# Kernel tuning notes

Measured on AMD Instinct MI355X. Metric: run time of the kernel, lower is better.

The kernel has to match this reference:

```python
import jax, jax.numpy as jnp
import numpy as np

N_HEADS = 32
N_KV_HEADS = 8
HEAD_DIM = 128  # hidden 4096 / 32
NEG_INF = -1e9


def _apply_rope(x, cos, sin):
    # x: [B, S, H, D]; cos/sin: [S, D//2] -> complex multiply on (even, odd) pairs
    B, S, H, D = x.shape
    xr = x.reshape(B, S, H, D // 2, 2)
    a, b = xr[..., 0], xr[..., 1]
    c = cos[None, :, None, :]
    s = sin[None, :, None, :]
    out = jnp.stack([a * c - b * s, a * s + b * c], axis=-1)
    return out.reshape(B, S, H, D)


def setup_inputs() -> dict:
    key = jax.random.key(0)
    ks = jax.random.split(key, 8)
    B, S, HID = 1, 2048, 4096
    hidden_states = jax.random.normal(ks[0], (B, S, HID), dtype=jnp.float32)
    # causal additive mask [1,1,S,S]
    causal = jnp.tril(jnp.ones((S, S), dtype=bool))
    attention_mask = jnp.where(causal, 0.0, NEG_INF).astype(jnp.float32)[None, None]
    # true rotary frequencies (theta=500000 as in llama3)
    half = HEAD_DIM // 2
    inv_freq = 1.0 / (500000.0 ** (np.arange(0, half, dtype=np.float32) / half))
    angles = np.arange(S, dtype=np.float32)[:, None] * inv_freq[None, :]
    freqs_cos = jnp.asarray(np.cos(angles), dtype=jnp.float32)
    freqs_sin = jnp.asarray(np.sin(angles), dtype=jnp.float32)
    sc = 0.02
    wq = jax.random.normal(ks[1], (HID, HID), dtype=jnp.float32) * sc
    wk = jax.random.normal(ks[2], (N_KV_HEADS * HEAD_DIM, HID), dtype=jnp.float32) * sc
    wv = jax.random.normal(ks[3], (N_KV_HEADS * HEAD_DIM, HID), dtype=jnp.float32) * sc
    wo = jax.random.normal(ks[4], (HID, HID), dtype=jnp.float32) * sc
    return {"hidden_states": hidden_states, "attention_mask": attention_mask,
            "freqs_cos": freqs_cos, "freqs_sin": freqs_sin,
            "wq": wq, "wk": wk, "wv": wv, "wo": wo}


def reference(hidden_states, attention_mask, freqs_cos, freqs_sin, wq, wk, wv, wo):
    B, S, HID = hidden_states.shape
    n_rep = N_HEADS // N_KV_HEADS
    # projections (torch Linear: x @ W.T)
    q = (hidden_states @ wq.T).reshape(B, S, N_HEADS, HEAD_DIM)
    k = (hidden_states @ wk.T).reshape(B, S, N_KV_HEADS, HEAD_DIM)
    v = (hidden_states @ wv.T).reshape(B, S, N_KV_HEADS, HEAD_DIM)
    # rotary on q (full cos/sin) and k
    q = _apply_rope(q, freqs_cos, freqs_sin)
    k = _apply_rope(k, freqs_cos, freqs_sin)
    # [B, H, S, D]
    q = q.transpose(0, 2, 1, 3)
    k = k.transpose(0, 2, 1, 3)
    v = v.transpose(0, 2, 1, 3)
    # GQA: repeat_interleave kv heads
    k = jnp.repeat(k, n_rep, axis=1)
    v = jnp.repeat(v, n_rep, axis=1)
    scores = jnp.einsum("bhqd,bhkd->bhqk", q, k) / jnp.sqrt(jnp.float32(HEAD_DIM))
    scores = scores + attention_mask
    probs = jax.nn.softmax(scores.astype(jnp.float32), axis=-1)
    attn = jnp.einsum("bhqk,bhkd->bhqd", probs, v)
    attn = attn.transpose(0, 2, 1, 3).reshape(B, S, N_HEADS * HEAD_DIM)
    return attn @ wo.T
```

## Files before the change

### kernel.cpp

```cpp
#include <hip/hip_runtime.h>
#include <hip/hip_bf16.h>
#include <math.h>

#define SEQ 2048
#define HID 4096
#define NH 32
#define NKV 8
#define HD 128
#define KVG (NH / NKV)
#define NQKV 6144

typedef __bf16 bf16x8 __attribute__((ext_vector_type(8)));
typedef float  f32x4  __attribute__((ext_vector_type(4)));

__device__ __forceinline__ unsigned short f2bf(float f) {
  union { float f; unsigned int u; } v; v.f = f;
  unsigned int r = v.u + 0x7FFFu + ((v.u >> 16) & 1u);
  return (unsigned short)(r >> 16);
}
__device__ __forceinline__ float bf2f(unsigned short h) {
  union { unsigned int u; float f; } v; v.u = ((unsigned int)h) << 16;
  return v.f;
}

__device__ __forceinline__ void glds16(const unsigned short* g, unsigned short* l) {
  __builtin_amdgcn_global_load_lds(
      (const __attribute__((address_space(1))) void*)g,
      (__attribute__((address_space(3))) void*)l, 16, 0, 0);
}

__global__ __launch_bounds__(256) void cvt_all(
    const float* __restrict__ H, const float* __restrict__ wq,
    const float* __restrict__ wk, const float* __restrict__ wv,
    const float* __restrict__ wo, unsigned short* __restrict__ ws)
{
  const long G1 = 1l << 20;
  const long M1 = 1l << 20;
  long g = (long)blockIdx.x * 256 + threadIdx.x;
  const float* src; unsigned short* dst; long rel;
  if      (g < 2 * G1) { src = H;  dst = ws;           rel = g;          }
  else if (g < 6 * G1) { src = wq; dst = ws + 8 * M1;  rel = g - 2 * G1; }
  else if (g < 7 * G1) { src = wk; dst = ws + 24 * M1; rel = g - 6 * G1; }
  else if (g < 8 * G1) { src = wv; dst = ws + 28 * M1; rel = g - 7 * G1; }
  else                 { src = wo; dst = ws + 32 * M1; rel = g - 8 * G1; }
  float4 v = ((const float4*)src)[rel];
  ushort4 o;
  o.x = f2bf(v.x); o.y = f2bf(v.y); o.z = f2bf(v.z); o.w = f2bf(v.w);
  ((ushort4*)dst)[rel] = o;
}

template<bool F32OUT>
__global__ __launch_bounds__(256) void gemm_nt(
    const unsigned short* __restrict__ A,
    const unsigned short* __restrict__ B,
    void* __restrict__ Cv,
    int M, int N, int K)
{
  __shared__ unsigned short As[128 * 64];
  __shared__ unsigned short Bs[128 * 64];
  const int t = threadIdx.x;
  const int lane = t & 63, wid = t >> 6;
  const int quad = lane >> 4, l16 = lane & 15;
  const int wm = (wid & 1) * 64, wn = (wid >> 1) * 64;
  const int m0 = blockIdx.y * 128, n0 = blockIdx.x * 128;

  int srow[4], sgch[4];
  const unsigned short* ga[4];
  const unsigned short* gb[4];
  unsigned short* la[4];
  unsigned short* lb[4];
  #pragma unroll
  for (int j = 0; j < 4; j++) {
    int pj = (wid * 4 + j) * 64 + lane;
    srow[j] = pj >> 3;
    sgch[j] = (pj & 7) ^ (srow[j] & 7);
    ga[j] = A + (size_t)(m0 + srow[j]) * K + sgch[j] * 8;
    gb[j] = B + (size_t)(n0 + srow[j]) * K + sgch[j] * 8;
    la[j] = &As[(wid * 4 + j) * 512];
    lb[j] = &Bs[(wid * 4 + j) * 512];
  }

  const f32x4 fzero = {0.f, 0.f, 0.f, 0.f};
  f32x4 acc[4][4];
  #pragma unroll
  for (int i = 0; i < 4; i++)
    #pragma unroll
    for (int j = 0; j < 4; j++) acc[i][j] = fzero;

  for (int k0 = 0; k0 < K; k0 += 64) {
    __syncthreads();
    #pragma unroll
    for (int j = 0; j < 4; j++) {
      glds16(ga[j], la[j]);
      glds16(gb[j], lb[j]);
      ga[j] += 64; gb[j] += 64;
    }
    __syncthreads();

    #pragma unroll
    for (int ks = 0; ks < 2; ks++) {
      bf16x8 af[4], bfr[4];
      #pragma unroll
      for (int mt = 0; mt < 4; mt++) {
        int row = wm + mt * 16 + l16;
        int cp = (ks * 4 + quad) ^ (l16 & 7);
        af[mt] = *(const bf16x8*)(&As[(row * 8 + cp) * 8]);
      }
      #pragma unroll
      for (int nt = 0; nt < 4; nt++) {
        int row = wn + nt * 16 + l16;
        int cp = (ks * 4 + quad) ^ (l16 & 7);
        bfr[nt] = *(const bf16x8*)(&Bs[(row * 8 + cp) * 8]);
      }
      #pragma unroll
      for (int mt = 0; mt < 4; mt++)
        #pragma unroll
        for (int nt = 0; nt < 4; nt++)
          acc[mt][nt] = __builtin_amdgcn_mfma_f32_16x16x32_bf16(af[mt], bfr[nt], acc[mt][nt], 0, 0, 0);
    }
  }

  #pragma unroll
  for (int mt = 0; mt < 4; mt++)
    #pragma unroll
    for (int nt = 0; nt < 4; nt++)
      #pragma unroll
      for (int r = 0; r < 4; r++) {
        int row = m0 + wm + mt * 16 + quad * 4 + r;
        int col = n0 + wn + nt * 16 + l16;
        float v = acc[mt][nt][r];
        if (F32OUT) ((float*)Cv)[(size_t)row * N + col] = v;
        else        ((unsigned short*)Cv)[(size_t)row * N + col] = f2bf(v);
      }
}

__global__ __launch_bounds__(256) void rope_vtrans(
    const unsigned short* __restrict__ QKVr,
    const float* __restrict__ cosT,
    const float* __restrict__ sinT,
    unsigned short* __restrict__ Qh,
    unsigned short* __restrict__ Kh,
    unsigned short* __restrict__ Vtg)
{
  __shared__ unsigned short T[64 * 66];
  int hh = blockIdx.y;
  int bx = blockIdx.x;
  int t = threadIdx.x;
  if (hh < NH + NKV) {
    int sub = t >> 6, d2 = t & 63;
    int s = bx * 4 + sub;
    float c = cosT[s * 64 + d2], sn = sinT[s * 64 + d2];
    if (hh < NH) {
      const unsigned short* src = QKVr + (size_t)s * NQKV + hh * HD;
      unsigned short* dst = Qh + ((size_t)hh * SEQ + s) * HD;
      float a = bf2f(src[2 * d2]), b = bf2f(src[2 * d2 + 1]);
      dst[2 * d2]     = f2bf(a * c - b * sn);
      dst[2 * d2 + 1] = f2bf(a * sn + b * c);
    } else {
      int h = hh - NH;
      const unsigned short* src = QKVr + (size_t)s * NQKV + HID + h * HD;
      unsigned short* dst = Kh + ((size_t)h * SEQ + s) * HD;
      float a = bf2f(src[2 * d2]), b = bf2f(src[2 * d2 + 1]);
      dst[2 * d2]     = f2bf(a * c - b * sn);
      dst[2 * d2 + 1] = f2bf(a * sn + b * c);
    }
  } else {
    int idx = bx >> 5;
    int kvh = idx >> 1, d0 = (idx & 1) * 64;
    int s0 = (bx & 31) * 64;
    int si = t >> 2, dchunk = t & 3;
    const unsigned short* src = QKVr + (size_t)(s0 + si) * NQKV + HID + NKV * HD + kvh * HD + d0 + dchunk * 16;
    uint4 a = *(const uint4*)src;
    uint4 b = *(const uint4*)(src + 8);
    unsigned int va[8] = {a.x, a.y, a.z, a.w, b.x, b.y, b.z, b.w};
    #pragma unroll
    for (int j = 0; j < 8; j++)
      *(unsigned int*)(&T[si * 66 + dchunk * 16 + j * 2]) = va[j];
    __syncthreads();
    int di = t >> 2, schunk = t & 3;
    unsigned short px[16];
    #pragma unroll
    for (int j = 0; j < 16; j++) px[j] = T[(schunk * 16 + j) * 66 + di];
    unsigned short* dst = Vtg + ((size_t)kvh * HD + d0 + di) * SEQ + s0 + schunk * 16;
    *(uint4*)dst = *(uint4*)px;
    *(uint4*)(dst + 8) = *(uint4*)(px + 8);
  }
}

__global__ __launch_bounds__(256) void flash_kernel(
    const unsigned short* __restrict__ Qh,
    const unsigned short* __restrict__ Kh,
    const unsigned short* __restrict__ Vtg,
    unsigned short* __restrict__ Obf)
{
  __shared__ unsigned short Ks[64 * 128];
  __shared__ unsigned short Vs[128 * 64];
  __shared__ unsigned short Ps[4][16 * 72];

  const int h = blockIdx.y;
  const int pairp = blockIdx.x;
  const int kvh = h / KVG;
  const int t = threadIdx.x;
  const int lane = t & 63, w = t >> 6;
  const int quad = lane >> 4, l16 = lane & 15;
  const float scale = 0.08838834764831845f;
  const float SHIFT = 8.0f;

  bf16x8 ones;
  #pragma unroll
  for (int j = 0; j < 8; j++) ones[j] = (__bf16)1.0f;

  int krow[4], kgch[4], vrow[4], vgch[4];
  unsigned short* lk[4];
  unsigned short* lv[4];
  #pragma unroll
  for (int j = 0; j < 4; j++) {
    int pj = (w * 4 + j) * 64 + lane;
    krow[j] = pj >> 4; kgch[j] = (pj & 15) ^ (krow[j] & 15);
    vrow[j] = pj >> 3; vgch[j] = (pj & 7) ^ (vrow[j] & 7);
    lk[j] = &Ks[(w * 4 + j) * 512];
    lv[j] = &Vs[(w * 4 + j) * 512];
  }

  unsigned short* Pw = Ps[w];
  const f32x4 fzero = {0.f, 0.f, 0.f, 0.f};

  #pragma unroll
  for (int pass = 0; pass < 2; pass++) {
    const int qt = pass ? (31 - pairp) : pairp;
    const int q0 = qt * 64;
    const int q = q0 + w * 16 + l16;

    bf16x8 aq[4];
    const unsigned short* Qp = Qh + ((size_t)h * SEQ + q0 + w * 16 + l16) * HD;
    #pragma unroll
    for (int ks = 0; ks < 4; ks++) aq[ks] = *(const bf16x8*)(Qp + ks * 32 + quad * 8);

    f32x4 o[8];
    #pragma unroll
    for (int dt = 0; dt < 8; dt++) o[dt] = fzero;
    f32x4 lacc = fzero;

    const unsigned short* gk[4];
    const unsigned short* gv[4];
    #pragma unroll
    for (int j = 0; j < 4; j++) {
      gk[j] = Kh + ((size_t)kvh * SEQ + krow[j]) * HD + kgch[j] * 8;
      gv[j] = Vtg + ((size_t)kvh * HD + vrow[j]) * SEQ + vgch[j] * 8;
    }

    for (int kv0 = 0; kv0 <= q0; kv0 += 64) {
      __syncthreads();
      #pragma unroll
      for (int j = 0; j < 4; j++) {
        glds16(gk[j], lk[j]);
        glds16(gv[j], lv[j]);
        gk[j] += 64 * HD;
        gv[j] += 64;
      }
      __syncthreads();

      f32x4 sc[4];
      #pragma unroll
      for (int kvt = 0; kvt < 4; kvt++) sc[kvt] = fzero;
      #pragma unroll
      for (int ks = 0; ks < 4; ks++)
        #pragma unroll
        for (int kvt = 0; kvt < 4; kvt++) {
          int row = kvt * 16 + l16;
          int cp = (ks * 4 + quad) ^ l16;
          bf16x8 bk = *(const bf16x8*)(&Ks[(row * 16 + cp) * 8]);
          sc[kvt] = __builtin_amdgcn_mfma_f32_16x16x32_bf16(bk, aq[ks], sc[kvt], 0, 0, 0);
        }

      #pragma unroll
      for (int kvt = 0; kvt < 4; kvt++) {
        unsigned short ph[4];
        #pragma unroll
        for (int r = 0; r < 4; r++) {
          int kv = kv0 + kvt * 16 + quad * 4 + r;
          float p = (kv > q) ? 0.f : __expf(fmaf(sc[kvt][r], scale, -SHIFT));
          ph[r] = f2bf(p);
        }
        *(uint2*)(&Pw[l16 * 72 + kvt * 16 + quad * 4]) = *(const uint2*)ph;
      }

      #pragma unroll
      for (int ks2 = 0; ks2 < 2; ks2++) {
        bf16x8 ap = *(const bf16x8*)(&Pw[l16 * 72 + ks2 * 32 + quad * 8]);
        lacc = __builtin_amdgcn_mfma_f32_16x16x32_bf16(ap, ones, lacc, 0, 0, 0);
        #pragma unroll
        for (int dt = 0; dt < 8; dt++) {
          int row = dt * 16 + l16;
          int cp = (ks2 * 4 + quad) ^ (l16 & 7);
          bf16x8 bv = *(const bf16x8*)(&Vs[(row * 8 + cp) * 8]);
          o[dt] = __builtin_amdgcn_mfma_f32_16x16x32_bf16(ap, bv, o[dt], 0, 0, 0);
        }
      }
    }

    #pragma unroll
    for (int dt = 0; dt < 8; dt++)
      #pragma unroll
      for (int r = 0; r < 4; r++) {
        int qq = q0 + w * 16 + quad * 4 + r;
        int d = dt * 16 + l16;
        Obf[(size_t)qq * HID + h * HD + d] = f2bf(o[dt][r] / lacc[r]);
      }
  }
}

extern "C" void kernel_launch(void* const* d_in, const int* in_sizes, int n_in,
                              void* d_out, int out_size, void* d_ws, size_t ws_size,
                              hipStream_t stream) {
  const float* H    = (const float*)d_in[0];
  const float* cosT = (const float*)d_in[2];
  const float* sinT = (const float*)d_in[3];
  const float* wq   = (const float*)d_in[4];
  const float* wk   = (const float*)d_in[5];
  const float* wv   = (const float*)d_in[6];
  const float* wo   = (const float*)d_in[7];

  unsigned short* ws = (unsigned short*)d_ws;
  const size_t M1 = 1u << 20;
  unsigned short* Hb   = ws;
  unsigned short* Wqkv = ws + (size_t)8  * M1;
  unsigned short* Wob  = ws + (size_t)32 * M1;
  unsigned short* QKVr = ws + (size_t)48 * M1;
  unsigned short* Qh   = ws + (size_t)8  * M1;
  unsigned short* Kh   = ws + (size_t)16 * M1;
  unsigned short* Vtg  = ws + (size_t)18 * M1;
  unsigned short* attn = ws;

  cvt_all<<<49152, 256, 0, stream>>>(H, wq, wk, wv, wo, ws);

  gemm_nt<false><<<dim3(48, 16), 256, 0, stream>>>(Hb, Wqkv, QKVr, SEQ, NQKV, HID);

  rope_vtrans<<<dim3(512, NH + NKV + 1), 256, 0, stream>>>(QKVr, cosT, sinT, Qh, Kh, Vtg);

  flash_kernel<<<dim3(16, NH), 256, 0, stream>>>(Qh, Kh, Vtg, attn);

  gemm_nt<true><<<dim3(32, 16), 256, 0, stream>>>(attn, Wob, d_out, SEQ, HID, HID);
}
```

Measured before the change: 482.6 us.

## Double-buffer GEMM LDS with 128x256 tiles and 8-wave ping-pong schedule

The NT GEMM now uses 512 threads and a 128x256 output tile. Its LDS is double-buffered: global-to-LDS loads for the next K-tiles are issued while MFMAs run on the current buffer, using split half-steps, explicit vmcnt waits, barriers and setprio. The aim is to hide global load latency that the old load-sync-compute loop exposed and to get more reuse per tile. In exchange it uses more LDS and launches fewer blocks (384 and 256), which could leave CUs underfilled on a 256-CU part. It also relies on hand-tuned waitcnt counts being correct.

```diff
diff --git a/kernel.cpp b/kernel.cpp
--- a/kernel.cpp
+++ b/kernel.cpp
@@ -50,35 +50,65 @@
 }
 
 template<bool F32OUT>
-__global__ __launch_bounds__(256) void gemm_nt(
+__global__ __launch_bounds__(512, 2) void gemm_nt(
     const unsigned short* __restrict__ A,
     const unsigned short* __restrict__ B,
     void* __restrict__ Cv,
     int M, int N, int K)
 {
-  __shared__ unsigned short As[128 * 64];
-  __shared__ unsigned short Bs[128 * 64];
+  __shared__ unsigned short As[2][128 * 64];
+  __shared__ unsigned short Bs[2][256 * 64];
   const int t = threadIdx.x;
   const int lane = t & 63, wid = t >> 6;
   const int quad = lane >> 4, l16 = lane & 15;
-  const int wm = (wid & 1) * 64, wn = (wid >> 1) * 64;
-  const int m0 = blockIdx.y * 128, n0 = blockIdx.x * 128;
-
-  int srow[4], sgch[4];
-  const unsigned short* ga[4];
-  const unsigned short* gb[4];
-  unsigned short* la[4];
-  unsigned short* lb[4];
-  #pragma unroll
-  for (int j = 0; j < 4; j++) {
-    int pj = (wid * 4 + j) * 64 + lane;
-    srow[j] = pj >> 3;
-    sgch[j] = (pj & 7) ^ (srow[j] & 7);
-    ga[j] = A + (size_t)(m0 + srow[j]) * K + sgch[j] * 8;
-    gb[j] = B + (size_t)(n0 + srow[j]) * K + sgch[j] * 8;
-    la[j] = &As[(wid * 4 + j) * 512];
-    lb[j] = &Bs[(wid * 4 + j) * 512];
-  }
+  const int wm = wid >> 2, wn = wid & 3;
+  const int m0 = blockIdx.y * 128, n0 = blockIdx.x * 256;
+  const int NT = K >> 6;
+
+  const int lrow8 = lane >> 3;
+  const int gch   = (lane & 7) ^ lrow8;
+
+  const int arb = (wid >> 2) * 64 + (wid & 3) * 8;
+  const unsigned short* gA[2];
+  unsigned short* lA[2][2];
+  #pragma unroll
+  for (int p = 0; p < 2; p++) {
+    int row = p * 32 + arb + lrow8;
+    gA[p] = A + (size_t)(m0 + row) * K + gch * 8;
+    lA[0][p] = &As[0][(p * 32 + arb) * 64];
+    lA[1][p] = &As[1][(p * 32 + arb) * 64];
+  }
+  const unsigned short* gB[2][2];
+  unsigned short* lB[2][2][2];
+  #pragma unroll
+  for (int p = 0; p < 2; p++)
+    #pragma unroll
+    for (int j = 0; j < 2; j++) {
+      int u = wid * 2 + j;
+      int rb = (u >> 2) * 64 + (u & 3) * 8;
+      int row = p * 32 + rb + lrow8;
+      gB[p][j] = B + (size_t)(n0 + row) * K + gch * 8;
+      lB[0][p][j] = &Bs[0][(p * 32 + rb) * 64];
+      lB[1][p][j] = &Bs[1][(p * 32 + rb) * 64];
+    }
+
+  auto stageA = [&](int p, int buf, int kt) {
+    glds16(gA[p] + (size_t)kt * 64, lA[buf][p]);
+  };
+  auto stageB = [&](int p, int buf, int kt) {
+    glds16(gB[p][0] + (size_t)kt * 64, lB[buf][p][0]);
+    glds16(gB[p][1] + (size_t)kt * 64, lB[buf][p][1]);
+  };
+  auto ldA = [&](int buf, int mt, int ks) -> bf16x8 {
+    int row = wm * 64 + mt * 16 + l16;
+    int cp = (ks * 4 + quad) ^ (l16 & 7);
+    return *(const bf16x8*)(&As[buf][row * 64 + cp * 8]);
+  };
+  auto ldB = [&](int buf, int nt, int ks) -> bf16x8 {
+    int row = wn * 64 + nt * 16 + l16;
+    int cp = (ks * 4 + quad) ^ (l16 & 7);
+    return *(const bf16x8*)(&Bs[buf][row * 64 + cp * 8]);
+  };
 
   const f32x4 fzero = {0.f, 0.f, 0.f, 0.f};
   f32x4 acc[4][4];
@@ -87,37 +117,61 @@
     #pragma unroll
     for (int j = 0; j < 4; j++) acc[i][j] = fzero;
 
-  for (int k0 = 0; k0 < K; k0 += 64) {
-    __syncthreads();
-    #pragma unroll
-    for (int j = 0; j < 4; j++) {
-      glds16(ga[j], la[j]);
-      glds16(gb[j], lb[j]);
-      ga[j] += 64; gb[j] += 64;
-    }
-    __syncthreads();
-
-    #pragma unroll
-    for (int ks = 0; ks < 2; ks++) {
-      bf16x8 af[4], bfr[4];
-      #pragma unroll
-      for (int mt = 0; mt < 4; mt++) {
-        int row = wm + mt * 16 + l16;
-        int cp = (ks * 4 + quad) ^ (l16 & 7);
-        af[mt] = *(const bf16x8*)(&As[(row * 8 + cp) * 8]);
-      }
-      #pragma unroll
-      for (int nt = 0; nt < 4; nt++) {
-        int row = wn + nt * 16 + l16;
-        int cp = (ks * 4 + quad) ^ (l16 & 7);
-        bfr[nt] = *(const bf16x8*)(&Bs[(row * 8 + cp) * 8]);
-      }
-      #pragma unroll
-      for (int mt = 0; mt < 4; mt++)
-        #pragma unroll
-        for (int nt = 0; nt < 4; nt++)
-          acc[mt][nt] = __builtin_amdgcn_mfma_f32_16x16x32_bf16(af[mt], bfr[nt], acc[mt][nt], 0, 0, 0);
-    }
+  stageA(0, 0, 0); stageB(0, 0, 0); stageB(1, 0, 0); stageA(1, 0, 0);
+  if (NT > 1) { stageA(0, 1, 1); stageB(0, 1, 1); stageB(1, 1, 1); }
+  asm volatile("s_waitcnt vmcnt(5)" ::: "memory");
+  __builtin_amdgcn_s_barrier();
+
+  for (int tt = 0; tt < NT; tt++) {
+    const int buf = tt & 1;
+
+    bf16x8 a0[2][2], bfr[4][2];
+    #pragma unroll
+    for (int mt = 0; mt < 2; mt++)
+      #pragma unroll
+      for (int ks = 0; ks < 2; ks++) a0[mt][ks] = ldA(buf, mt, ks);
+    #pragma unroll
+    for (int nt = 0; nt < 4; nt++)
+      #pragma unroll
+      for (int ks = 0; ks < 2; ks++) bfr[nt][ks] = ldB(buf, nt, ks);
+    if (tt + 1 < NT) stageA(1, (tt + 1) & 1, tt + 1);
+    __builtin_amdgcn_s_barrier();
+    asm volatile("s_waitcnt lgkmcnt(0)" ::: "memory");
+    __builtin_amdgcn_s_setprio(1);
+    #pragma unroll
+    for (int mt = 0; mt < 2; mt++)
+      #pragma unroll
+      for (int nt = 0; nt < 4; nt++)
+        #pragma unroll
+        for (int ks = 0; ks < 2; ks++)
+          acc[mt][nt] = __builtin_amdgcn_mfma_f32_16x16x32_bf16(a0[mt][ks], bfr[nt][ks], acc[mt][nt], 0, 0, 0);
+    __builtin_amdgcn_s_setprio(0);
+    __builtin_amdgcn_s_barrier();
+
+    bf16x8 a1[2][2];
+    #pragma unroll
+    for (int mt = 0; mt < 2; mt++)
+      #pragma unroll
+      for (int ks = 0; ks < 2; ks++) a1[mt][ks] = ldA(buf, 2 + mt, ks);
+    if (tt + 2 < NT) {
+      stageA(0, buf, tt + 2);
+      stageB(0, buf, tt + 2);
+      stageB(1, buf, tt + 2);
+    }
+    __builtin_amdgcn_s_barrier();
+    asm volatile("s_waitcnt lgkmcnt(0)" ::: "memory");
+    __builtin_amdgcn_s_setprio(1);
+    #pragma unroll
+    for (int mt = 0; mt < 2; mt++)
+      #pragma unroll
+      for (int nt = 0; nt < 4; nt++)
+        #pragma unroll
+        for (int ks = 0; ks < 2; ks++)
+          acc[2 + mt][nt] = __builtin_amdgcn_mfma_f32_16x16x32_bf16(a1[mt][ks], bfr[nt][ks], acc[2 + mt][nt], 0, 0, 0);
+    __builtin_amdgcn_s_setprio(0);
+    if (tt + 2 < NT) asm volatile("s_waitcnt vmcnt(5)" ::: "memory");
+    else             asm volatile("s_waitcnt vmcnt(0)" ::: "memory");
+    __builtin_amdgcn_s_barrier();
   }
 
   #pragma unroll
@@ -126,8 +180,8 @@
     for (int nt = 0; nt < 4; nt++)
       #pragma unroll
       for (int r = 0; r < 4; r++) {
-        int row = m0 + wm + mt * 16 + quad * 4 + r;
-        int col = n0 + wn + nt * 16 + l16;
+        int row = m0 + wm * 64 + mt * 16 + quad * 4 + r;
+        int col = n0 + wn * 64 + nt * 16 + l16;
         float v = acc[mt][nt][r];
         if (F32OUT) ((float*)Cv)[(size_t)row * N + col] = v;
         else        ((unsigned short*)Cv)[(size_t)row * N + col] = f2bf(v);
@@ -334,11 +388,11 @@
 
   cvt_all<<<49152, 256, 0, stream>>>(H, wq, wk, wv, wo, ws);
 
-  gemm_nt<false><<<dim3(48, 16), 256, 0, stream>>>(Hb, Wqkv, QKVr, SEQ, NQKV, HID);
+  gemm_nt<false><<<dim3(24, 16), 512, 0, stream>>>(Hb, Wqkv, QKVr, SEQ, NQKV, HID);
 
   rope_vtrans<<<dim3(512, NH + NKV + 1), 256, 0, stream>>>(QKVr, cosT, sinT, Qh, Kh, Vtg);
 
   flash_kernel<<<dim3(16, NH), 256, 0, stream>>>(Qh, Kh, Vtg, attn);
 
-  gemm_nt<true><<<dim3(32, 16), 256, 0, stream>>>(attn, Wob, d_out, SEQ, HID, HID);
-}
+  gemm_nt<true><<<dim3(16, 16), 512, 0, stream>>>(attn, Wob, d_out, SEQ, HID, HID);
+}
```

After: 528.9 us. 9.6% more time.

## Add 256x192 double-buffered ping-pong GEMM for QKV projection

Applied to the files above, without the earlier changes.

Swaps the generic 128x128 QKV GEMM for a dedicated kernel with 256x192 tiles, 512 threads and 8 waves. It double-buffers LDS and interleaves async global-to-LDS loads with MFMA phases, using explicit waitcnt, barriers and setprio. The grid becomes 256 blocks (32x8), which fits the CU count more evenly and gives more reuse per tile. The cost is heavy LDS use (about 112KB) and many barriers, which may limit occupancy and make the kernel fragile.

```diff
diff --git a/kernel.cpp b/kernel.cpp
--- a/kernel.cpp
+++ b/kernel.cpp
@@ -28,6 +28,8 @@
       (const __attribute__((address_space(1))) void*)g,
       (__attribute__((address_space(3))) void*)l, 16, 0, 0);
 }
+
+#define MFMA_BF16 __builtin_amdgcn_mfma_f32_16x16x32_bf16
 
 __global__ __launch_bounds__(256) void cvt_all(
     const float* __restrict__ H, const float* __restrict__ wq,
@@ -49,6 +51,211 @@
   ((ushort4*)dst)[rel] = o;
 }
 
+__global__ __launch_bounds__(512, 2) void gemm_qkv(
+    const unsigned short* __restrict__ A,
+    const unsigned short* __restrict__ B,
+    unsigned short* __restrict__ C,
+    int M, int N, int K)
+{
+  __shared__ unsigned short As[2][256 * 64];
+  __shared__ unsigned short Bs[2][192 * 64];
+  const int t = threadIdx.x;
+  const int lane = t & 63, wid = t >> 6;
+  const int quad = lane >> 4, l16 = lane & 15;
+  const int wm = wid >> 2, wn = wid & 3;
+  const int m0 = blockIdx.y * 256, n0 = blockIdx.x * 192;
+  const int U = K >> 7;
+  const int lrow8 = lane >> 3;
+  const int gch = (lane & 7) ^ lrow8;
+
+  const unsigned short* gA[4];
+  const unsigned short* gB[3];
+  #pragma unroll
+  for (int ua = 0; ua < 4; ua++)
+    gA[ua] = A + (size_t)(m0 + ua * 64 + wid * 8 + lrow8) * K + gch * 8;
+  #pragma unroll
+  for (int ub = 0; ub < 3; ub++)
+    gB[ub] = B + (size_t)(n0 + ub * 64 + wid * 8 + lrow8) * K + gch * 8;
+
+  auto stA = [&](int ua, int buf, int kt) {
+    glds16(gA[ua] + (size_t)kt * 64, &As[buf][(ua * 64 + wid * 8) * 64]);
+  };
+  auto stB = [&](int ub, int buf, int kt) {
+    glds16(gB[ub] + (size_t)kt * 64, &Bs[buf][(ub * 64 + wid * 8) * 64]);
+  };
+  auto ldA = [&](int buf, int mt, int ks) -> bf16x8 {
+    int row = wm * 128 + mt * 16 + l16;
+    int cp = (ks * 4 + quad) ^ (l16 & 7);
+    return *(const bf16x8*)(&As[buf][row * 64 + cp * 8]);
+  };
+  auto ldB = [&](int buf, int nt, int ks) -> bf16x8 {
+    int row = wn * 48 + nt * 16 + l16;
+    int cp = (ks * 4 + quad) ^ (l16 & 7);
+    return *(const bf16x8*)(&Bs[buf][row * 64 + cp * 8]);
+  };
+
+  const f32x4 fzero = {0.f, 0.f, 0.f, 0.f};
+  f32x4 acc[8][3];
+  #pragma unroll
+  for (int i = 0; i < 8; i++)
+    #pragma unroll
+    for (int j = 0; j < 3; j++) acc[i][j] = fzero;
+
+  #pragma unroll
+  for (int ua = 0; ua < 4; ua++) stA(ua, 0, 0);
+  #pragma unroll
+  for (int ub = 0; ub < 3; ub++) stB(ub, 0, 0);
+  stB(0, 1, 1); stB(1, 1, 1); stB(2, 1, 1);
+  stA(0, 1, 1); stA(2, 1, 1); stA(1, 1, 1);
+  asm volatile("s_waitcnt vmcnt(6)" ::: "memory");
+  __builtin_amdgcn_s_barrier();
+
+  bf16x8 fa[4][2], fb[3][2];
+
+  for (int u = 0; u < U; u++) {
+    const bool last = (u == U - 1);
+    const int k1 = 2 * u + 1, k2 = 2 * u + 2, k3 = 2 * u + 3;
+
+    #pragma unroll
+    for (int mt = 0; mt < 4; mt++)
+      #pragma unroll
+      for (int ks = 0; ks < 2; ks++) fa[mt][ks] = ldA(0, mt, ks);
+    #pragma unroll
+    for (int nt = 0; nt < 3; nt++)
+      #pragma unroll
+      for (int ks = 0; ks < 2; ks++) fb[nt][ks] = ldB(0, nt, ks);
+    stA(3, 1, k1);
+    __builtin_amdgcn_s_barrier();
+    asm volatile("s_waitcnt lgkmcnt(0)" ::: "memory");
+    __builtin_amdgcn_s_setprio(1);
+    #pragma unroll
+    for (int mt = 0; mt < 4; mt++)
+      #pragma unroll
+      for (int nt = 0; nt < 2; nt++)
+        #pragma unroll
+        for (int ks = 0; ks < 2; ks++)
+          acc[mt][nt] = MFMA_BF16(fa[mt][ks], fb[nt][ks], acc[mt][nt], 0, 0, 0);
+    __builtin_amdgcn_s_setprio(0);
+    __builtin_amdgcn_s_barrier();
+
+    if (!last) { stB(0, 0, k2); stB(1, 0, k2); }
+    __builtin_amdgcn_s_barrier();
+    __builtin_amdgcn_s_setprio(1);
+    #pragma unroll
+    for (int mt = 0; mt < 4; mt++)
+      #pragma unroll
+      for (int ks = 0; ks < 2; ks++)
+        acc[mt][2] = MFMA_BF16(fa[mt][ks], fb[2][ks], acc[mt][2], 0, 0, 0);
+    __builtin_amdgcn_s_setprio(0);
+    __builtin_amdgcn_s_barrier();
+
+    #pragma unroll
+    for (int mt = 0; mt < 4; mt++)
+      #pragma unroll
+      for (int ks = 0; ks < 2; ks++) fa[mt][ks] = ldA(0, 4 + mt, ks);
+    if (!last) { stB(2, 0, k2); stA(0, 0, k2); }
+    __builtin_amdgcn_s_barrier();
+    asm volatile("s_waitcnt lgkmcnt(0)" ::: "memory");
+    __builtin_amdgcn_s_setprio(1);
+    #pragma unroll
+    for (int mt = 0; mt < 4; mt++)
+      #pragma unroll
+      for (int nt = 0; nt < 2; nt++)
+        #pragma unroll
+        for (int ks = 0; ks < 2; ks++)
+          acc[4 + mt][nt] = MFMA_BF16(fa[mt][ks], fb[nt][ks], acc[4 + mt][nt], 0, 0, 0);
+    __builtin_amdgcn_s_setprio(0);
+    __builtin_amdgcn_s_barrier();
+
+    if (!last) { stA(2, 0, k2); stA(1, 0, k2); }
+    __builtin_amdgcn_s_barrier();
+    __builtin_amdgcn_s_setprio(1);
+    #pragma unroll
+    for (int mt = 0; mt < 4; mt++)
+      #pragma unroll
+      for (int ks = 0; ks < 2; ks++)
+        acc[4 + mt][2] = MFMA_BF16(fa[mt][ks], fb[2][ks], acc[4 + mt][2], 0, 0, 0);
+    __builtin_amdgcn_s_setprio(0);
+    if (!last) asm volatile("s_waitcnt vmcnt(6)" ::: "memory");
+    else       asm volatile("s_waitcnt vmcnt(0)" ::: "memory");
+    __builtin_amdgcn_s_barrier();
+
+    #pragma unroll
+    for (int mt = 0; mt < 4; mt++)
+      #pragma unroll
+      for (int ks = 0; ks < 2; ks++) fa[mt][ks] = ldA(1, mt, ks);
+    #pragma unroll
+    for (int nt = 0; nt < 3; nt++)
+      #pragma unroll
+      for (int ks = 0; ks < 2; ks++) fb[nt][ks] = ldB(1, nt, ks);
+    if (!last) stA(3, 0, k2);
+    __builtin_amdgcn_s_barrier();
+    asm volatile("s_waitcnt lgkmcnt(0)" ::: "memory");
+    __builtin_amdgcn_s_setprio(1);
+    #pragma unroll
+    for (int mt = 0; mt < 4; mt++)
+      #pragma unroll
+      for (int nt = 0; nt < 2; nt++)
+        #pragma unroll
+        for (int ks = 0; ks < 2; ks++)
+          acc[mt][nt] = MFMA_BF16(fa[mt][ks], fb[nt][ks], acc[mt][nt], 0, 0, 0);
+    __builtin_amdgcn_s_setprio(0);
+    __builtin_amdgcn_s_barrier();
+
+    if (!last) { stB(0, 1, k3); stB(1, 1, k3); }
+    __builtin_amdgcn_s_barrier();
+    __builtin_amdgcn_s_setprio(1);
+    #pragma unroll
+    for (int mt = 0; mt < 4; mt++)
+      #pragma unroll
+      for (int ks = 0; ks < 2; ks++)
+        acc[mt][2] = MFMA_BF16(fa[mt][ks], fb[2][ks], acc[mt][2], 0, 0, 0);
+    __builtin_amdgcn_s_setprio(0);
+    __builtin_amdgcn_s_barrier();
+
+    #pragma unroll
+    for (int mt = 0; mt < 4; mt++)
+      #pragma unroll
+      for (int ks = 0; ks < 2; ks++) fa[mt][ks] = ldA(1, 4 + mt, ks);
+    if (!last) { stB(2, 1, k3); stA(0, 1, k3); }
+    __builtin_amdgcn_s_barrier();
+    asm volatile("s_waitcnt lgkmcnt(0)" ::: "memory");
+    __builtin_amdgcn_s_setprio(1);
+    #pragma unroll
+    for (int mt = 0; mt < 4; mt++)
+      #pragma unroll
+      for (int nt = 0; nt < 2; nt++)
+        #pragma unroll
+        for (int ks = 0; ks < 2; ks++)
+          acc[4 + mt][nt] = MFMA_BF16(fa[mt][ks], fb[nt][ks], acc[4 + mt][nt], 0, 0, 0);
+    __builtin_amdgcn_s_setprio(0);
+    __builtin_amdgcn_s_barrier();
+
+    if (!last) { stA(2, 1, k3); stA(1, 1, k3); }
+    __builtin_amdgcn_s_barrier();
+    __builtin_amdgcn_s_setprio(1);
+    #pragma unroll
+    for (int mt = 0; mt < 4; mt++)
+      #pragma unroll
+      for (int ks = 0; ks < 2; ks++)
+        acc[4 + mt][2] = MFMA_BF16(fa[mt][ks], fb[2][ks], acc[4 + mt][2], 0, 0, 0);
+    __builtin_amdgcn_s_setprio(0);
+    if (!last) asm volatile("s_waitcnt vmcnt(6)" ::: "memory");
+    __builtin_amdgcn_s_barrier();
+  }
+
+  #pragma unroll
+  for (int mt = 0; mt < 8; mt++)
+    #pragma unroll
+    for (int nt = 0; nt < 3; nt++)
+      #pragma unroll
+      for (int r = 0; r < 4; r++) {
+        int row = m0 + wm * 128 + mt * 16 + quad * 4 + r;
+        int col = n0 + wn * 48 + nt * 16 + l16;
+        C[(size_t)row * N + col] = f2bf(acc[mt][nt][r]);
+      }
+}
+
 template<bool F32OUT>
 __global__ __launch_bounds__(256) void gemm_nt(
     const unsigned short* __restrict__ A,
@@ -116,7 +323,7 @@
       for (int mt = 0; mt < 4; mt++)
         #pragma unroll
         for (int nt = 0; nt < 4; nt++)
-          acc[mt][nt] = __builtin_amdgcn_mfma_f32_16x16x32_bf16(af[mt], bfr[nt], acc[mt][nt], 0, 0, 0);
+          acc[mt][nt] = MFMA_BF16(af[mt], bfr[nt], acc[mt][nt], 0, 0, 0);
     }
   }
 
@@ -270,7 +477,7 @@
           int row = kvt * 16 + l16;
           int cp = (ks * 4 + quad) ^ l16;
           bf16x8 bk = *(const bf16x8*)(&Ks[(row * 16 + cp) * 8]);
-          sc[kvt] = __builtin_amdgcn_mfma_f32_16x16x32_bf16(bk, aq[ks], sc[kvt], 0, 0, 0);
+          sc[kvt] = MFMA_BF16(bk, aq[ks], sc[kvt], 0, 0, 0);
         }
 
       #pragma unroll
@@ -288,13 +495,13 @@
       #pragma unroll
       for (int ks2 = 0; ks2 < 2; ks2++) {
         bf16x8 ap = *(const bf16x8*)(&Pw[l16 * 72 + ks2 * 32 + quad * 8]);
-        lacc = __builtin_amdgcn_mfma_f32_16x16x32_bf16(ap, ones, lacc, 0, 0, 0);
+        lacc = MFMA_BF16(ap, ones, lacc, 0, 0, 0);
         #pragma unroll
         for (int dt = 0; dt < 8; dt++) {
           int row = dt * 16 + l16;
           int cp = (ks2 * 4 + quad) ^ (l16 & 7);
           bf16x8 bv = *(const bf16x8*)(&Vs[(row * 8 + cp) * 8]);
-          o[dt] = __builtin_amdgcn_mfma_f32_16x16x32_bf16(ap, bv, o[dt], 0, 0, 0);
+          o[dt] = MFMA_BF16(ap, bv, o[dt], 0, 0, 0);
         }
       }
     }
@@ -334,7 +541,7 @@
 
   cvt_all<<<49152, 256, 0, stream>>>(H, wq, wk, wv, wo, ws);
 
-  gemm_nt<false><<<dim3(48, 16), 256, 0, stream>>>(Hb, Wqkv, QKVr, SEQ, NQKV, HID);
+  gemm_qkv<<<dim3(32, 8), 512, 0, stream>>>(Hb, Wqkv, QKVr, SEQ, NQKV, HID);
 
   rope_vtrans<<<dim3(512, NH + NKV + 1), 256, 0, stream>>>(QKVr, cosT, sinT, Qh, Kh, Vtg);
 
```

Result: no change. 487.5 us (+1.0%).

## Double-buffer K/V tiles in flash attention with async prefetch and setprio

Applied to the files above, without the earlier changes.

The flash attention kernel now keeps two LDS buffers for the K and V tiles. It issues the global-to-LDS loads for the next KV tile before computing on the current one, waiting only with a partial vmcnt so the loads overlap the MFMA work. It also raises wave priority around the MFMA sections and replaces the two full syncthreads per iteration with explicit barriers. The cost is roughly double the LDS used for K/V, which may cut the number of resident blocks per CU.

```diff
diff --git a/kernel.cpp b/kernel.cpp
--- a/kernel.cpp
+++ b/kernel.cpp
@@ -28,6 +28,8 @@
       (const __attribute__((address_space(1))) void*)g,
       (__attribute__((address_space(3))) void*)l, 16, 0, 0);
 }
+
+#define MFMA_BF16 __builtin_amdgcn_mfma_f32_16x16x32_bf16
 
 __global__ __launch_bounds__(256) void cvt_all(
     const float* __restrict__ H, const float* __restrict__ wq,
@@ -116,7 +118,7 @@
       for (int mt = 0; mt < 4; mt++)
         #pragma unroll
         for (int nt = 0; nt < 4; nt++)
-          acc[mt][nt] = __builtin_amdgcn_mfma_f32_16x16x32_bf16(af[mt], bfr[nt], acc[mt][nt], 0, 0, 0);
+          acc[mt][nt] = MFMA_BF16(af[mt], bfr[nt], acc[mt][nt], 0, 0, 0);
     }
   }
 
@@ -193,8 +195,8 @@
     const unsigned short* __restrict__ Vtg,
     unsigned short* __restrict__ Obf)
 {
-  __shared__ unsigned short Ks[64 * 128];
-  __shared__ unsigned short Vs[128 * 64];
+  __shared__ unsigned short Ks[2][64 * 128];
+  __shared__ unsigned short Vs[2][128 * 64];
   __shared__ unsigned short Ps[4][16 * 72];
 
   const int h = blockIdx.y;
@@ -211,16 +213,25 @@
   for (int j = 0; j < 8; j++) ones[j] = (__bf16)1.0f;
 
   int krow[4], kgch[4], vrow[4], vgch[4];
-  unsigned short* lk[4];
-  unsigned short* lv[4];
   #pragma unroll
   for (int j = 0; j < 4; j++) {
     int pj = (w * 4 + j) * 64 + lane;
     krow[j] = pj >> 4; kgch[j] = (pj & 15) ^ (krow[j] & 15);
     vrow[j] = pj >> 3; vgch[j] = (pj & 7) ^ (vrow[j] & 7);
-    lk[j] = &Ks[(w * 4 + j) * 512];
-    lv[j] = &Vs[(w * 4 + j) * 512];
-  }
+  }
+
+  const unsigned short* Kbase = Kh + (size_t)kvh * SEQ * HD;
+  const unsigned short* Vbase = Vtg + (size_t)kvh * HD * SEQ;
+
+  auto stage = [&](int buf, int kv0) {
+    #pragma unroll
+    for (int j = 0; j < 4; j++) {
+      glds16(Kbase + (size_t)(kv0 + krow[j]) * HD + kgch[j] * 8,
+             &Ks[buf][(w * 4 + j) * 512]);
+      glds16(Vbase + (size_t)vrow[j] * SEQ + kv0 + vgch[j] * 8,
+             &Vs[buf][(w * 4 + j) * 512]);
+    }
+  };
 
   unsigned short* Pw = Ps[w];
   const f32x4 fzero = {0.f, 0.f, 0.f, 0.f};
@@ -241,37 +252,37 @@
     for (int dt = 0; dt < 8; dt++) o[dt] = fzero;
     f32x4 lacc = fzero;
 
-    const unsigned short* gk[4];
-    const unsigned short* gv[4];
-    #pragma unroll
-    for (int j = 0; j < 4; j++) {
-      gk[j] = Kh + ((size_t)kvh * SEQ + krow[j]) * HD + kgch[j] * 8;
-      gv[j] = Vtg + ((size_t)kvh * HD + vrow[j]) * SEQ + vgch[j] * 8;
-    }
-
-    for (int kv0 = 0; kv0 <= q0; kv0 += 64) {
-      __syncthreads();
-      #pragma unroll
-      for (int j = 0; j < 4; j++) {
-        glds16(gk[j], lk[j]);
-        glds16(gv[j], lv[j]);
-        gk[j] += 64 * HD;
-        gv[j] += 64;
-      }
-      __syncthreads();
+    const int nIt = (q0 >> 6) + 1;
+    stage(0, 0);
+
+    for (int it = 0; it < nIt; it++) {
+      const int buf = it & 1;
+      const int kv0 = it << 6;
+      if (it + 1 < nIt) {
+        stage(buf ^ 1, kv0 + 64);
+        asm volatile("s_waitcnt vmcnt(8)" ::: "memory");
+      } else {
+        asm volatile("s_waitcnt vmcnt(0)" ::: "memory");
+      }
+      __builtin_amdgcn_s_barrier();
+
+      const unsigned short* Kb = Ks[buf];
+      const unsigned short* Vb = Vs[buf];
 
       f32x4 sc[4];
       #pragma unroll
       for (int kvt = 0; kvt < 4; kvt++) sc[kvt] = fzero;
+      __builtin_amdgcn_s_setprio(1);
       #pragma unroll
       for (int ks = 0; ks < 4; ks++)
         #pragma unroll
         for (int kvt = 0; kvt < 4; kvt++) {
           int row = kvt * 16 + l16;
           int cp = (ks * 4 + quad) ^ l16;
-          bf16x8 bk = *(const bf16x8*)(&Ks[(row * 16 + cp) * 8]);
-          sc[kvt] = __builtin_amdgcn_mfma_f32_16x16x32_bf16(bk, aq[ks], sc[kvt], 0, 0, 0);
+          bf16x8 bk = *(const bf16x8*)(&Kb[(row * 16 + cp) * 8]);
+          sc[kvt] = MFMA_BF16(bk, aq[ks], sc[kvt], 0, 0, 0);
         }
+      __builtin_amdgcn_s_setprio(0);
 
       #pragma unroll
       for (int kvt = 0; kvt < 4; kvt++) {
@@ -285,18 +296,21 @@
         *(uint2*)(&Pw[l16 * 72 + kvt * 16 + quad * 4]) = *(const uint2*)ph;
       }
 
+      __builtin_amdgcn_s_setprio(1);
       #pragma unroll
       for (int ks2 = 0; ks2 < 2; ks2++) {
         bf16x8 ap = *(const bf16x8*)(&Pw[l16 * 72 + ks2 * 32 + quad * 8]);
-        lacc = __builtin_amdgcn_mfma_f32_16x16x32_bf16(ap, ones, lacc, 0, 0, 0);
+        lacc = MFMA_BF16(ap, ones, lacc, 0, 0, 0);
         #pragma unroll
         for (int dt = 0; dt < 8; dt++) {
           int row = dt * 16 + l16;
           int cp = (ks2 * 4 + quad) ^ (l16 & 7);
-          bf16x8 bv = *(const bf16x8*)(&Vs[(row * 8 + cp) * 8]);
-          o[dt] = __builtin_amdgcn_mfma_f32_16x16x32_bf16(ap, bv, o[dt], 0, 0, 0);
+          bf16x8 bv = *(const bf16x8*)(&Vb[(row * 8 + cp) * 8]);
+          o[dt] = MFMA_BF16(ap, bv, o[dt], 0, 0, 0);
         }
       }
+      __builtin_amdgcn_s_setprio(0);
+      __builtin_amdgcn_s_barrier();
     }
 
     #pragma unroll
```

Result: no change. 482.5 us (-0.0%).
